# Optimization experiments

Hardware: AMD Instinct MI355X
Metric: run time of the kernel (lower is better)

## Reference

```python
import jax, jax.numpy as jnp
import numpy as np

B, T, C, HS = 4, 2048, 1024, 128

def setup_inputs() -> dict:
    key = jax.random.key(0)
    k0, k1, k2, k3 = jax.random.split(key, 4)
    scale = 1.0 / np.sqrt(C)
    return {
        "x": jax.random.normal(k0, (B, T, C), dtype=jnp.float32),
        "Wk": jax.random.normal(k1, (C, HS), dtype=jnp.float32) * scale,
        "Wq": jax.random.normal(k2, (C, HS), dtype=jnp.float32) * scale,
        "Wv": jax.random.normal(k3, (C, HS), dtype=jnp.float32) * scale,
    }

def reference(x, Wk, Wq, Wv):
    # k, q, v: [B, T, HS]
    k = jnp.einsum('btc,ch->bth', x, Wk)
    q = jnp.einsum('btc,ch->bth', x, Wq)
    v = jnp.einsum('btc,ch->bth', x, Wv)
    hs = k.shape[-1]
    # full T x T scores (no causal mask in source), scaled by head_size**-0.5
    wei = jnp.einsum('bqh,bkh->bqk', q, k) * (hs ** -0.5)
    wei = jax.nn.softmax(wei, axis=-1)
    # dropout p=0.0 -> identity
    out = jnp.einsum('bqk,bkh->bqh', wei, v)
    return out
```

## Files before the change

### kernel.cpp

```cpp
#include <hip/hip_runtime.h>
#include <hip/hip_bf16.h>

typedef float  f32x4  __attribute__((ext_vector_type(4)));
typedef float  f32x8  __attribute__((ext_vector_type(8)));
typedef float  f32x16 __attribute__((ext_vector_type(16)));
typedef short  s8v    __attribute__((ext_vector_type(8)));
typedef __bf16 b8v    __attribute__((ext_vector_type(8)));
typedef unsigned int u32;
typedef unsigned short ushort;

#define T_DIM  2048
#define C_DIM  1024


typedef const __attribute__((address_space(1))) u32 gu32;
typedef __attribute__((address_space(3))) u32 lu32;

static __device__ __forceinline__ void glds16(const void* g, void* l) {
  __builtin_amdgcn_global_load_lds((gu32*)g, (lu32*)l, 16, 0, 0);
}

static __device__ __forceinline__ b8v ldb8(const ushort* p) {
  return __builtin_bit_cast(b8v, *reinterpret_cast<const s8v*>(p));
}

static __device__ __forceinline__ b8v cvt8(f32x8 v) {
  b8v r;
#pragma unroll
  for (int i = 0; i < 8; ++i) r[i] = (__bf16)v[i];
  return r;
}

static __device__ __forceinline__ ushort bfu(float f) {
  __bf16 h = (__bf16)f;
  return __builtin_bit_cast(ushort, h);
}

static __device__ __forceinline__ f32x16 mfma32(b8v a, b8v b, f32x16 c) {
  return __builtin_amdgcn_mfma_f32_32x32x16_bf16(a, b, c, 0, 0, 0);
}

#define BAR_VM(N)                                                        \
  asm volatile("s_waitcnt vmcnt(" #N ") lgkmcnt(0)" ::: "memory");       \
  __builtin_amdgcn_s_barrier();                                          \
  asm volatile("" ::: "memory");

__global__ __launch_bounds__(256) void wconv(const float* __restrict__ Wq,
                                             const float* __restrict__ Wk,
                                             const float* __restrict__ Wv,
                                             ushort* __restrict__ Wt) {
  __shared__ float lds[32][65];
  const int m  = blockIdx.z;
  const int c0 = blockIdx.x * 32;
  const int h0 = blockIdx.y * 64;
  const float* W = (m == 0) ? Wq : (m == 1) ? Wk : Wv;

  const int cl = threadIdx.x >> 3;
  const int h8 = (threadIdx.x & 7) * 8;
  {
    float4 a = *reinterpret_cast<const float4*>(W + (c0 + cl) * 128 + h0 + h8);
    float4 b =
        *reinterpret_cast<const float4*>(W + (c0 + cl) * 128 + h0 + h8 + 4);
    lds[cl][h8] = a.x; lds[cl][h8 + 1] = a.y;
    lds[cl][h8 + 2] = a.z; lds[cl][h8 + 3] = a.w;
    lds[cl][h8 + 4] = b.x; lds[cl][h8 + 5] = b.y;
    lds[cl][h8 + 6] = b.z; lds[cl][h8 + 7] = b.w;
  }
  __syncthreads();
  const int hl = threadIdx.x >> 2;
  const int cs = (threadIdx.x & 3) * 8;
  s8v o;
#pragma unroll
  for (int i = 0; i < 8; ++i) o[i] = (short)bfu(lds[cs + i][hl]);
  *reinterpret_cast<s8v*>(Wt + (m * 128 + h0 + hl) * C_DIM + c0 + cs) = o;
}

__global__ __launch_bounds__(256) void proj(const float* __restrict__ x,
                                            const ushort* __restrict__ Wt,
                                            ushort* __restrict__ q,
                                            ushort* __restrict__ k,
                                            ushort* __restrict__ vt) {
  __shared__ __align__(16) ushort Ab[2][32 * 72];
  __shared__ __align__(16) ushort Bb[2][128 * 64];
  __shared__ __align__(16) ushort stage[5120];

  const int t   = threadIdx.x;
  const int w   = t >> 6;
  const int lid = t & 63;
  const int hi  = lid >> 5;
  const int ln  = lid & 31;
  const int m   = blockIdx.y;
  const int r0  = blockIdx.x * 32;

  const int arow = t >> 3;
  const int acol = (t & 7) * 8;
  const float* ag = x + (r0 + arow) * C_DIM + acol;

  const int bswz = (((lid & 7) ^ (lid >> 3)) << 4);
  const char* bg = (const char*)(Wt + m * 128 * C_DIM);

  f32x16 acc[2] = {};

#pragma unroll
  for (int j = 0; j < 4; ++j) {
    int h = j * 32 + w * 8 + (lid >> 3);
    glds16(bg + h * 2048 + bswz, (char*)&Bb[0][0] + j * 4096 + w * 1024);
  }
  {
    f32x8 av = *reinterpret_cast<const f32x8*>(ag);
    b8v ac = cvt8(av);
    *reinterpret_cast<s8v*>(&Ab[0][arow * 72 + acol]) =
        __builtin_bit_cast(s8v, ac);
  }
  __syncthreads();

  int cur = 0;
#pragma unroll 1
  for (int i = 0; i < 16; ++i) {
    const int nxt = cur ^ 1;
    f32x8 an;
    if (i < 15) {
      const int kk = (i + 1) * 64;
#pragma unroll
      for (int j = 0; j < 4; ++j) {
        int h = j * 32 + w * 8 + (lid >> 3);
        glds16(bg + h * 2048 + kk * 2 + bswz,
               (char*)&Bb[nxt][0] + j * 4096 + w * 1024);
      }
      an = *reinterpret_cast<const f32x8*>(ag + kk);
    }

    const int h = w * 32 + ln;
#pragma unroll
    for (int s = 0; s < 4; ++s) {
      b8v af = ldb8(&Ab[cur][ln * 72 + s * 16 + hi * 8]);
      int inner = ((s * 2 + hi) << 4) ^ ((h & 7) << 4);
      b8v bf = ldb8((const ushort*)((const char*)&Bb[cur][h * 64] + inner));
      __builtin_amdgcn_s_setprio(1);
      acc[s & 1] = mfma32(af, bf, acc[s & 1]);
      __builtin_amdgcn_s_setprio(0);
    }

    if (i < 15) {
      b8v anc = cvt8(an);
      *reinterpret_cast<s8v*>(&Ab[nxt][arow * 72 + acol]) =
          __builtin_bit_cast(s8v, anc);
    }
    __syncthreads();
    cur = nxt;
  }

  f32x16 fa = acc[0] + acc[1];

  if (m < 2) {
#pragma unroll
    for (int r = 0; r < 16; ++r) {
      int row = (r & 3) + 8 * (r >> 2) + 4 * hi;
      stage[row * 136 + w * 32 + ln] = bfu(fa[r]);
    }
    __syncthreads();
    ushort* dst = (m == 0) ? q : k;
#pragma unroll
    for (int c = 0; c < 2; ++c) {
      int chunk = c * 256 + t;
      int row = chunk >> 4, col8 = chunk & 15;
      s8v v8 = *reinterpret_cast<const s8v*>(&stage[row * 136 + col8 * 8]);
      *reinterpret_cast<s8v*>(&dst[(r0 + row) * 128 + col8 * 8]) = v8;
    }
  } else {
#pragma unroll
    for (int r = 0; r < 16; ++r) {
      int trow = (r & 3) + 8 * (r >> 2) + 4 * hi;
      stage[(w * 32 + ln) * 40 + trow] = bfu(fa[r]);
    }
    __syncthreads();
    int b = blockIdx.x >> 6;
    int tbase = (blockIdx.x & 63) * 32;
#pragma unroll
    for (int c = 0; c < 2; ++c) {
      int chunk = c * 256 + t;
      int h2 = chunk >> 2, t8 = chunk & 3;
      s8v v8 = *reinterpret_cast<const s8v*>(&stage[h2 * 40 + t8 * 8]);
      *reinterpret_cast<s8v*>(&vt[(b * 128 + h2) * T_DIM + tbase + t8 * 8]) =
          v8;
    }
  }
}

#define ATTN_STAGE(KV0, BUF)                                              \
  _Pragma("unroll") for (int j = 0; j < 4; ++j) {                         \
    int row = w * 16 + j * 4 + (lid >> 4);                                \
    int p_ = (row >> 2) & 7;                                              \
    int pg = (p_ & 4) | ((p_ & 1) << 1) | ((p_ >> 1) & 1);                \
    int srow = (row & ~31) | (pg << 2) | (row & 3);                       \
    glds16(kgb + ((KV0) + srow) * 256 + (((lid & 15) ^ (row & 15)) << 4), \
           smem + (BUF) * 65536 + w * 4096 + j * 1024);                   \
  }                                                                       \
  _Pragma("unroll") for (int j = 0; j < 4; ++j) {                         \
    int h = w * 16 + j * 4 + (lid >> 4);                                  \
    glds16(vgb + h * 4096 + (KV0) * 2 + (((lid & 15) ^ (h & 15)) << 4),   \
           smem + (BUF) * 65536 + 32768 + w * 4096 + j * 1024);           \
  }

__global__ __launch_bounds__(512) void attn2(const ushort* __restrict__ q,
                                             const ushort* __restrict__ k,
                                             const ushort* __restrict__ vt,
                                             float* __restrict__ out,
                                             float* __restrict__ parts,
                                             float* __restrict__ lps) {
  extern __shared__ __align__(16) char smem[];

  const int t   = threadIdx.x;
  const int w   = t >> 6;
  const int lid = t & 63;
  const int hi  = lid >> 5;
  const int ln  = lid & 31;
  const int wq  = w >> 2;
  const int wk  = w & 3;

  const int id = blockIdx.x;
  const int g  = id & 7;
  const int b  = g >> 1;
  const int z  = g & 1;
  const int t0 = (id >> 3) * 64;

  const ushort* qp = q + (b * T_DIM + t0 + wq * 32) * 128;
  b8v aq[8];
#pragma unroll
  for (int s = 0; s < 8; ++s)
    aq[s] = ldb8(&qp[ln * 128 + s * 16 + hi * 8]);

  const char* kgb = (const char*)(k + b * T_DIM * 128);
  const char* vgb = (const char*)(vt + b * 128 * T_DIM);
  const int kv_base = z * 1024;

  const int R = wk * 32 + ln;
  int koff[8];
#pragma unroll
  for (int s = 0; s < 8; ++s)
    koff[s] = R * 256 + (((s * 2 + hi) ^ (R & 15)) << 4);
  int voff[4][2];
#pragma unroll
  for (int ht = 0; ht < 4; ++ht)
#pragma unroll
    for (int s = 0; s < 2; ++s) {
      int Hrow = ht * 32 + ln;
      int chunk = wk * 4 + s * 2 + hi;
      voff[ht][s] = 32768 + Hrow * 256 + ((chunk ^ (Hrow & 15)) << 4);
    }

  f32x16 of[4] = {};
  float lsum = 0.0f;
  const float scale = 0.08838834764831845f;

#define ATTN2_BODY(BUF)                                                  \
  {                                                                      \
    const char* Tb = smem + (BUF) * 65536;                               \
    b8v kfr[8];                                                          \
    _Pragma("unroll") for (int s = 0; s < 8; ++s)                        \
        kfr[s] = ldb8((const ushort*)(Tb + koff[s]));                    \
    f32x16 S = {};                                                       \
    __builtin_amdgcn_s_setprio(1);                                       \
    _Pragma("unroll") for (int s = 0; s < 8; ++s)                        \
        S = mfma32(kfr[s], aq[s], S);                                    \
    __builtin_amdgcn_s_setprio(0);                                       \
    float p[16];                                                         \
    _Pragma("unroll") for (int r = 0; r < 16; ++r) {                     \
      p[r] = __expf(S[r] * scale - 4.0f);                                \
      lsum += p[r];                                                      \
    }                                                                    \
    b8v pk0, pk1;                                                        \
    _Pragma("unroll") for (int r = 0; r < 8; ++r) {                      \
      pk0[r] = (__bf16)p[r];                                             \
      pk1[r] = (__bf16)p[8 + r];                                         \
    }                                                                    \
    __builtin_amdgcn_s_setprio(1);                                       \
    _Pragma("unroll") for (int ht = 0; ht < 4; ++ht) {                   \
      b8v v0 = ldb8((const ushort*)(Tb + voff[ht][0]));                  \
      b8v v1 = ldb8((const ushort*)(Tb + voff[ht][1]));                  \
      of[ht] = mfma32(pk0, v0, of[ht]);                                  \
      of[ht] = mfma32(pk1, v1, of[ht]);                                  \
    }                                                                    \
    __builtin_amdgcn_s_setprio(0);                                       \
  }

  ATTN_STAGE(kv_base, 0)

#pragma unroll 1
  for (int i = 0; i < 8; ++i) {
    BAR_VM(0)
    if (i < 7) { ATTN_STAGE(kv_base + (i + 1) * 128, (i + 1) & 1) }
    ATTN2_BODY(i & 1)
  }
#undef ATTN2_BODY

  lsum += __shfl_xor(lsum, 32);

  __syncthreads();

  float* ob = (float*)smem;
  float* lb = (float*)(smem + 98304);

  if (lid < 32) lb[(wq * 4 + wk) * 32 + lid] = lsum;
  if (wk != 0) {
#pragma unroll
    for (int ht = 0; ht < 4; ++ht)
#pragma unroll
      for (int r = 0; r < 16; ++r) {
        int qm = (r & 3) + 8 * (r >> 2) + 4 * hi;
        ob[((wk - 1) * 64 + wq * 32 + qm) * 128 + ht * 32 + ln] = of[ht][r];
      }
  }
  __syncthreads();
  if (wk == 0) {
    float* dsto = (z == 0) ? out : parts;
#pragma unroll
    for (int ht = 0; ht < 4; ++ht)
#pragma unroll
      for (int r = 0; r < 16; ++r) {
        int qm = (r & 3) + 8 * (r >> 2) + 4 * hi;
        int row = wq * 32 + qm;
        int col = ht * 32 + ln;
        float val = of[ht][r] + ob[(0 * 64 + row) * 128 + col] +
                    ob[(1 * 64 + row) * 128 + col] +
                    ob[(2 * 64 + row) * 128 + col];
        dsto[(b * T_DIM + t0 + row) * 128 + col] = val;
      }
    if (lid < 32) {
      float lt = lb[(wq * 4 + 0) * 32 + lid] + lb[(wq * 4 + 1) * 32 + lid] +
                 lb[(wq * 4 + 2) * 32 + lid] + lb[(wq * 4 + 3) * 32 + lid];
      lps[z * 8192 + b * T_DIM + t0 + wq * 32 + lid] = lt;
    }
  }
}

__global__ __launch_bounds__(256) void fin(float* __restrict__ out,
                                           const float* __restrict__ parts,
                                           const float* __restrict__ lps) {
  int tid = blockIdx.x * 256 + threadIdx.x;
  int idx = tid * 4;
  int row = idx >> 7;
  float inv = 1.0f / (lps[row] + lps[8192 + row]);
  f32x4 a = *reinterpret_cast<const f32x4*>(out + idx);
  f32x4 c = *reinterpret_cast<const f32x4*>(parts + idx);
  f32x4 r;
#pragma unroll
  for (int i = 0; i < 4; ++i) r[i] = (a[i] + c[i]) * inv;
  *reinterpret_cast<f32x4*>(out + idx) = r;
}

extern "C" void kernel_launch(void* const* d_in, const int* in_sizes, int n_in,
                              void* d_out, int out_size, void* d_ws,
                              size_t ws_size, hipStream_t stream) {
  const float* x  = (const float*)d_in[0];
  const float* Wk = (const float*)d_in[1];
  const float* Wq = (const float*)d_in[2];
  const float* Wv = (const float*)d_in[3];
  float* out = (float*)d_out;

  char* ws = (char*)d_ws;
  ushort* Wt  = (ushort*)ws;
  ushort* qb  = (ushort*)(ws + (1u << 20));
  ushort* kb  = (ushort*)(ws + 3u * (1u << 20));
  ushort* vtb = (ushort*)(ws + 5u * (1u << 20));
  float* parts = (float*)(ws + 8u * (1u << 20));
  float* lps   = (float*)(ws + 12u * (1u << 20));

  (void)hipFuncSetAttribute(reinterpret_cast<const void*>(&attn2),
                            hipFuncAttributeMaxDynamicSharedMemorySize, 131072);

  wconv<<<dim3(32, 2, 3), dim3(256), 0, stream>>>(Wq, Wk, Wv, Wt);
  proj<<<dim3(256, 3), dim3(256), 0, stream>>>(x, Wt, qb, kb, vtb);
  attn2<<<dim3(256), dim3(512), 131072, stream>>>(qb, kb, vtb, out,
                                                  parts, lps);
  fin<<<dim3(1024), dim3(256), 0, stream>>>(out, parts, lps);
}
```

Measured before the change: 48.91 us.

## Split projection K-loop across 8 waves with LDS reduction, reuse Bb for staging

The projection kernel now runs 512 threads per block. The 8 waves split into two K-halves across 4 column groups, and each wave does 2 MFMAs per step instead of 4. Partial accumulators are then summed through LDS, and the separate staging buffer is replaced by aliasing the B double-buffer, which cuts LDS use. The aim is more waves in flight to hide load latency in the projection, at the cost of an extra reduction pass and barriers.

```diff
diff --git a/kernel.cpp b/kernel.cpp
--- a/kernel.cpp
+++ b/kernel.cpp
@@ -4,7 +4,9 @@
 typedef float  f32x4  __attribute__((ext_vector_type(4)));
 typedef float  f32x8  __attribute__((ext_vector_type(8)));
 typedef float  f32x16 __attribute__((ext_vector_type(16)));
+typedef short  s4v    __attribute__((ext_vector_type(4)));
 typedef short  s8v    __attribute__((ext_vector_type(8)));
+typedef __bf16 b4v    __attribute__((ext_vector_type(4)));
 typedef __bf16 b8v    __attribute__((ext_vector_type(8)));
 typedef unsigned int u32;
 typedef unsigned short ushort;
@@ -24,10 +26,10 @@
   return __builtin_bit_cast(b8v, *reinterpret_cast<const s8v*>(p));
 }
 
-static __device__ __forceinline__ b8v cvt8(f32x8 v) {
-  b8v r;
-#pragma unroll
-  for (int i = 0; i < 8; ++i) r[i] = (__bf16)v[i];
+static __device__ __forceinline__ b4v cvt4(f32x4 v) {
+  b4v r;
+#pragma unroll
+  for (int i = 0; i < 4; ++i) r[i] = (__bf16)v[i];
   return r;
 }
 
@@ -75,25 +77,28 @@
   *reinterpret_cast<s8v*>(Wt + (m * 128 + h0 + hl) * C_DIM + c0 + cs) = o;
 }
 
-__global__ __launch_bounds__(256) void proj(const float* __restrict__ x,
+__global__ __launch_bounds__(512) void proj(const float* __restrict__ x,
                                             const ushort* __restrict__ Wt,
                                             ushort* __restrict__ q,
                                             ushort* __restrict__ k,
                                             ushort* __restrict__ vt) {
   __shared__ __align__(16) ushort Ab[2][32 * 72];
   __shared__ __align__(16) ushort Bb[2][128 * 64];
-  __shared__ __align__(16) ushort stage[5120];
+  float* red = (float*)&Bb[0][0];
+  ushort* stage = &Bb[1][0];
 
   const int t   = threadIdx.x;
   const int w   = t >> 6;
   const int lid = t & 63;
   const int hi  = lid >> 5;
   const int ln  = lid & 31;
+  const int ks  = w >> 2;
+  const int nc  = w & 3;
   const int m   = blockIdx.y;
   const int r0  = blockIdx.x * 32;
 
-  const int arow = t >> 3;
-  const int acol = (t & 7) * 8;
+  const int arow = t >> 4;
+  const int acol = (t & 15) * 4;
   const float* ag = x + (r0 + arow) * C_DIM + acol;
 
   const int bswz = (((lid & 7) ^ (lid >> 3)) << 4);
@@ -101,16 +106,19 @@
 
   f32x16 acc[2] = {};
 
-#pragma unroll
-  for (int j = 0; j < 4; ++j) {
-    int h = j * 32 + w * 8 + (lid >> 3);
-    glds16(bg + h * 2048 + bswz, (char*)&Bb[0][0] + j * 4096 + w * 1024);
-  }
+#define PROJ_BSTAGE(KK, BUF)                                              \
+  _Pragma("unroll") for (int j = 0; j < 2; ++j) {                         \
+    int h = j * 64 + w * 8 + (lid >> 3);                                  \
+    glds16(bg + h * 2048 + (KK) * 2 + bswz,                               \
+           (char*)&Bb[BUF][0] + j * 8192 + w * 1024);                     \
+  }
+
+  f32x4 av = *reinterpret_cast<const f32x4*>(ag);
+  PROJ_BSTAGE(0, 0)
   {
-    f32x8 av = *reinterpret_cast<const f32x8*>(ag);
-    b8v ac = cvt8(av);
-    *reinterpret_cast<s8v*>(&Ab[0][arow * 72 + acol]) =
-        __builtin_bit_cast(s8v, ac);
+    b4v ac = cvt4(av);
+    *reinterpret_cast<s4v*>(&Ab[0][arow * 72 + acol]) =
+        __builtin_bit_cast(s4v, ac);
   }
   __syncthreads();
 
@@ -118,72 +126,79 @@
 #pragma unroll 1
   for (int i = 0; i < 16; ++i) {
     const int nxt = cur ^ 1;
-    f32x8 an;
+    f32x4 an;
     if (i < 15) {
       const int kk = (i + 1) * 64;
-#pragma unroll
-      for (int j = 0; j < 4; ++j) {
-        int h = j * 32 + w * 8 + (lid >> 3);
-        glds16(bg + h * 2048 + kk * 2 + bswz,
-               (char*)&Bb[nxt][0] + j * 4096 + w * 1024);
-      }
-      an = *reinterpret_cast<const f32x8*>(ag + kk);
-    }
-
-    const int h = w * 32 + ln;
-#pragma unroll
-    for (int s = 0; s < 4; ++s) {
+      PROJ_BSTAGE(kk, nxt)
+      an = *reinterpret_cast<const f32x4*>(ag + kk);
+    }
+
+    const int h = nc * 32 + ln;
+#pragma unroll
+    for (int c = 0; c < 2; ++c) {
+      const int s = ks * 2 + c;
       b8v af = ldb8(&Ab[cur][ln * 72 + s * 16 + hi * 8]);
       int inner = ((s * 2 + hi) << 4) ^ ((h & 7) << 4);
-      b8v bf = ldb8((const ushort*)((const char*)&Bb[cur][h * 64] + inner));
+      b8v bf =
+          ldb8((const ushort*)((const char*)&Bb[cur][0] + h * 128 + inner));
       __builtin_amdgcn_s_setprio(1);
-      acc[s & 1] = mfma32(af, bf, acc[s & 1]);
+      acc[c] = mfma32(af, bf, acc[c]);
       __builtin_amdgcn_s_setprio(0);
     }
 
     if (i < 15) {
-      b8v anc = cvt8(an);
-      *reinterpret_cast<s8v*>(&Ab[nxt][arow * 72 + acol]) =
-          __builtin_bit_cast(s8v, anc);
+      b4v anc = cvt4(an);
+      *reinterpret_cast<s4v*>(&Ab[nxt][arow * 72 + acol]) =
+          __builtin_bit_cast(s4v, anc);
     }
     __syncthreads();
     cur = nxt;
   }
+#undef PROJ_BSTAGE
 
   f32x16 fa = acc[0] + acc[1];
 
+  if (ks == 1) {
+#pragma unroll
+    for (int r = 0; r < 16; ++r) {
+      int qm = (r & 3) + 8 * (r >> 2) + 4 * hi;
+      red[(nc * 32 + qm) * 32 + ln] = fa[r];
+    }
+  }
+  __syncthreads();
+  if (ks == 0) {
+#pragma unroll
+    for (int r = 0; r < 16; ++r) {
+      int qm = (r & 3) + 8 * (r >> 2) + 4 * hi;
+      fa[r] += red[(nc * 32 + qm) * 32 + ln];
+    }
+    if (m < 2) {
+#pragma unroll
+      for (int r = 0; r < 16; ++r) {
+        int row = (r & 3) + 8 * (r >> 2) + 4 * hi;
+        stage[row * 136 + nc * 32 + ln] = bfu(fa[r]);
+      }
+    } else {
+#pragma unroll
+      for (int r = 0; r < 16; ++r) {
+        int trow = (r & 3) + 8 * (r >> 2) + 4 * hi;
+        stage[(nc * 32 + ln) * 40 + trow] = bfu(fa[r]);
+      }
+    }
+  }
+  __syncthreads();
+
   if (m < 2) {
-#pragma unroll
-    for (int r = 0; r < 16; ++r) {
-      int row = (r & 3) + 8 * (r >> 2) + 4 * hi;
-      stage[row * 136 + w * 32 + ln] = bfu(fa[r]);
-    }
-    __syncthreads();
     ushort* dst = (m == 0) ? q : k;
-#pragma unroll
-    for (int c = 0; c < 2; ++c) {
-      int chunk = c * 256 + t;
-      int row = chunk >> 4, col8 = chunk & 15;
-      s8v v8 = *reinterpret_cast<const s8v*>(&stage[row * 136 + col8 * 8]);
-      *reinterpret_cast<s8v*>(&dst[(r0 + row) * 128 + col8 * 8]) = v8;
-    }
+    int row = t >> 4, col8 = t & 15;
+    s8v v8 = *reinterpret_cast<const s8v*>(&stage[row * 136 + col8 * 8]);
+    *reinterpret_cast<s8v*>(&dst[(r0 + row) * 128 + col8 * 8]) = v8;
   } else {
-#pragma unroll
-    for (int r = 0; r < 16; ++r) {
-      int trow = (r & 3) + 8 * (r >> 2) + 4 * hi;
-      stage[(w * 32 + ln) * 40 + trow] = bfu(fa[r]);
-    }
-    __syncthreads();
     int b = blockIdx.x >> 6;
     int tbase = (blockIdx.x & 63) * 32;
-#pragma unroll
-    for (int c = 0; c < 2; ++c) {
-      int chunk = c * 256 + t;
-      int h2 = chunk >> 2, t8 = chunk & 3;
-      s8v v8 = *reinterpret_cast<const s8v*>(&stage[h2 * 40 + t8 * 8]);
-      *reinterpret_cast<s8v*>(&vt[(b * 128 + h2) * T_DIM + tbase + t8 * 8]) =
-          v8;
-    }
+    int h2 = t >> 2, t8 = t & 3;
+    s8v v8 = *reinterpret_cast<const s8v*>(&stage[h2 * 40 + t8 * 8]);
+    *reinterpret_cast<s8v*>(&vt[(b * 128 + h2) * T_DIM + tbase + t8 * 8]) = v8;
   }
 }
 
@@ -370,7 +385,7 @@
                             hipFuncAttributeMaxDynamicSharedMemorySize, 131072);
 
   wconv<<<dim3(32, 2, 3), dim3(256), 0, stream>>>(Wq, Wk, Wv, Wt);
-  proj<<<dim3(256, 3), dim3(256), 0, stream>>>(x, Wt, qb, kb, vtb);
+  proj<<<dim3(256, 3), dim3(512), 0, stream>>>(x, Wt, qb, kb, vtb);
   attn2<<<dim3(256), dim3(512), 131072, stream>>>(qb, kb, vtb, out,
                                                   parts, lps);
   fin<<<dim3(1024), dim3(256), 0, stream>>>(out, parts, lps);
```

Result: no change. 48.05 us, median of 3 (-1.8%).
